# Optimization experiments

Hardware: AMD Instinct MI355X
Metric: run time of the kernel (lower is better)

Reference implementation:

```python
import jax, jax.numpy as jnp
import numpy as np

H = 16  # num_heads
NEG = -1.0e9


def setup_inputs() -> dict:
    key = jax.random.key(0)
    ks = jax.random.split(key, 12)
    B, Q, D, S = 2, 2048, 1024, 512
    sc = 0.02
    return {
        "main_input": jax.random.normal(ks[0], (B, Q, D), jnp.float32),
        "side_input": jax.random.normal(ks[1], (S, D), jnp.float32),
        "att_mask": jax.random.randint(ks[2], (B, Q, Q + S), 0, 2, jnp.int32),
        "Wq": jax.random.normal(ks[3], (D, D), jnp.float32) * sc,
        "bq": jnp.zeros((D,), jnp.float32),
        "Wk": jax.random.normal(ks[4], (D, D), jnp.float32) * sc,
        "bk": jnp.zeros((D,), jnp.float32),
        "Wv": jax.random.normal(ks[5], (D, D), jnp.float32) * sc,
        "bv": jnp.zeros((D,), jnp.float32),
        "Wo": jax.random.normal(ks[6], (D, D), jnp.float32) * sc,
        "bo": jnp.zeros((D,), jnp.float32),
    }


def _heads(x, W, b):
    # x: [..., D] -> [..., H, d]
    y = x @ W + b
    return y.reshape(y.shape[:-1] + (H, y.shape[-1] // H))


def reference(main_input, side_input, att_mask, Wq, bq, Wk, bk, Wv, bv, Wo, bo):
    B, Q, D = main_input.shape
    S = side_input.shape[0]
    d = D // H
    q = _heads(main_input, Wq, bq)          # [B,Q,H,d]
    k = _heads(main_input, Wk, bk)          # [B,Q,H,d]
    v = _heads(main_input, Wv, bv)          # [B,Q,H,d]
    sk = _heads(side_input, Wk, bk)         # [S,H,d] (shared projections)
    sv = _heads(side_input, Wv, bv)         # [S,H,d]
    scores_main = jnp.einsum('bqhd,bkhd->bhqk', q, k)
    scores_side = jnp.einsum('bqhd,khd->bhqk', q, sk)
    scores = jnp.concatenate([scores_main, scores_side], axis=3)  # [B,H,Q,Q+S]
    scores = scores / jnp.sqrt(jnp.asarray(d, scores.dtype))
    adder = NEG * (1.0 - att_mask.astype(scores.dtype))[:, None, :, :]
    probs = jax.nn.softmax(scores + adder, axis=-1)
    out_main = jnp.einsum('bhqk,bkhd->bqhd', probs[..., :Q], v)
    out_side = jnp.einsum('bhqk,khd->bqhd', probs[..., Q:], sv)
    att = (out_main + out_side).reshape(B, Q, D)
    return att @ Wo + bo
```

## Files before the change

### kernel.cpp

```cpp
#include <hip/hip_runtime.h>
#include <cstdint>

typedef short s16x8 __attribute__((ext_vector_type(8)));
typedef short s16x4 __attribute__((ext_vector_type(4)));
typedef unsigned short u16x4 __attribute__((ext_vector_type(4)));
typedef float f32x4 __attribute__((ext_vector_type(4)));
typedef float f32x16 __attribute__((ext_vector_type(16)));
typedef unsigned int u32x4 __attribute__((ext_vector_type(4)));

#define ND 1024
#define NH 16
#define DH 64
#define NQ 2048
#define NL 2560
#define MMAIN 4096
#define MCAT 4608
#define Q_SCALE 0.18033688011112042f

__device__ __forceinline__ unsigned short f2b(float f) {
  unsigned u = __builtin_bit_cast(unsigned, f);
  u += 0x7FFFu + ((u >> 16) & 1u);
  return (unsigned short)(u >> 16);
}

__device__ __forceinline__ void gload16(const void* g, void* l) {
  __builtin_amdgcn_global_load_lds(
      (const __attribute__((address_space(1))) void*)(unsigned long long)(uintptr_t)g,
      (__attribute__((address_space(3))) void*)(unsigned)(uintptr_t)l,
      16, 0, 0);
}

__device__ __forceinline__ f32x4 mfma16(s16x8 a, s16x8 b, f32x4 c) {
  return __builtin_amdgcn_mfma_f32_16x16x32_bf16(a, b, c, 0, 0, 0);
}
__device__ __forceinline__ f32x16 mfma32(s16x8 a, s16x8 b, f32x16 c) {
  return __builtin_amdgcn_mfma_f32_32x32x16_bf16(a, b, c, 0, 0, 0);
}

__device__ __forceinline__ float exp2r(float x) {
  float r;
  asm("v_exp_f32 %0, %1" : "=v"(r) : "v"(x));
  return r;
}

__device__ __forceinline__ int sext_bit(unsigned w, int c) {
#if __has_builtin(__builtin_amdgcn_sbfe)
  return __builtin_amdgcn_sbfe((int)w, c, 1);
#else
  return -(int)((w >> c) & 1u);
#endif
}

__device__ __forceinline__ unsigned cvt_pk_bf16(float lo, float hi) {
  unsigned d;
  asm("v_cvt_pk_bf16_f32 %0, %1, %2" : "=v"(d) : "v"(lo), "v"(hi));
  return d;
}

__device__ __forceinline__ void plane32_swap(unsigned& a, unsigned& b) {
  asm("v_permlane32_swap_b32 %0, %1" : "+v"(a), "+v"(b));
}

__device__ __forceinline__ f32x16 z16() {
  f32x16 v;
#pragma unroll
  for (int i = 0; i < 16; ++i) v[i] = 0.f;
  return v;
}


__global__ __launch_bounds__(256) void k_prep(const float* __restrict__ mainp,
                                              const float* __restrict__ sidep,
                                              const int* __restrict__ mask,
                                              const float* __restrict__ W0,
                                              const float* __restrict__ W1,
                                              const float* __restrict__ W2,
                                              const float* __restrict__ W3,
                                              short* __restrict__ xcat,
                                              short* __restrict__ Wt,
                                              unsigned* __restrict__ pm) {
  __shared__ float T[64][65];
  const int bid = blockIdx.x;
  const int tid = threadIdx.x;
  if (bid < 4608) {
    size_t i4 = ((size_t)bid * 256 + tid) * 4;
    const float* src =
        (i4 < (size_t)MMAIN * ND) ? (mainp + i4) : (sidep + (i4 - (size_t)MMAIN * ND));
    float4 v = *(const float4*)src;
    s16x4 o;
    o[0] = (short)f2b(v.x); o[1] = (short)f2b(v.y);
    o[2] = (short)f2b(v.z); o[3] = (short)f2b(v.w);
    *(s16x4*)(xcat + i4) = o;
  } else if (bid < 4608 + 1024) {
    const int id = bid - 4608;
    const int z = id >> 8, rem = id & 255;
    const float* W = z == 0 ? W0 : z == 1 ? W1 : z == 2 ? W2 : W3;
    short* out = Wt + (size_t)z * (ND * ND);
    const int r = tid >> 2, c0 = (tid & 3) * 16;
    const int k0 = (rem & 15) * 64, n0 = (rem >> 4) * 64;
#pragma unroll
    for (int i = 0; i < 4; ++i) {
      float4 v = *(const float4*)(W + (size_t)(k0 + r) * ND + n0 + c0 + i * 4);
      T[r][c0 + i * 4 + 0] = v.x; T[r][c0 + i * 4 + 1] = v.y;
      T[r][c0 + i * 4 + 2] = v.z; T[r][c0 + i * 4 + 3] = v.w;
    }
    __syncthreads();
    s16x8 o0, o1;
#pragma unroll
    for (int i = 0; i < 8; ++i) o0[i] = (short)f2b(T[c0 + i][r]);
#pragma unroll
    for (int i = 0; i < 8; ++i) o1[i] = (short)f2b(T[c0 + 8 + i][r]);
    *(s16x8*)(out + (size_t)(n0 + r) * ND + k0 + c0) = o0;
    *(s16x8*)(out + (size_t)(n0 + r) * ND + k0 + c0 + 8) = o1;
  } else {
    const int W = (bid - 5632) * 256 + tid;
    const int4* src = (const int4*)(mask + (size_t)W * 32);
    unsigned bits = 0;
#pragma unroll
    for (int i = 0; i < 8; ++i) {
      int4 v = src[i];
      bits |= (unsigned)(v.x & 1) << (i * 4 + 0);
      bits |= (unsigned)(v.y & 1) << (i * 4 + 1);
      bits |= (unsigned)(v.z & 1) << (i * 4 + 2);
      bits |= (unsigned)(v.w & 1) << (i * 4 + 3);
    }
    pm[W] = bits;
  }
}


__global__ __launch_bounds__(256) void k_gemm_qkv(const short* __restrict__ A,
                                                  const short* __restrict__ Bt,
                                                  const float* __restrict__ bqp,
                                                  const float* __restrict__ bkp,
                                                  const float* __restrict__ bvp,
                                                  short* __restrict__ qb,
                                                  short* __restrict__ kb,
                                                  short* __restrict__ vt) {
  __shared__ __align__(16) short As[128 * 64];
  __shared__ __align__(16) short Bs[128 * 64];
  const int tid = threadIdx.x;
  const int w = tid >> 6, l = tid & 63;
  const int lg = l >> 4, li = l & 15;
  const int wr = w >> 1, wc = w & 1;
  const int fid = blockIdx.x + 24 * blockIdx.y;
  const int rid = (fid & 7) * 108 + (fid >> 3);
  const int m0 = (rid / 24) * 128, n0 = (rid % 24) * 128;

  f32x4 acc[4][4];
#pragma unroll
  for (int i = 0; i < 4; ++i)
#pragma unroll
    for (int j = 0; j < 4; ++j) acc[i][j] = (f32x4){0.f, 0.f, 0.f, 0.f};

  const int cb = (l & 7) ^ (l >> 3);
  const int rsub = l >> 3;

  for (int kt = 0; kt < 16; ++kt) {
    __syncthreads();
#pragma unroll
    for (int i = 0; i < 4; ++i) {
      int c = w * 4 + i;
      int rr = c * 8 + rsub;
      gload16(A + (size_t)(m0 + rr) * ND + kt * 64 + cb * 8, As + c * 512);
      gload16(Bt + (size_t)(n0 + rr) * ND + kt * 64 + cb * 8, Bs + c * 512);
    }
    __syncthreads();
#pragma unroll
    for (int kk = 0; kk < 2; ++kk) {
      const int blk = (((kk * 4) + lg) ^ (l & 7)) * 8;
      s16x8 af[4], bf[4];
#pragma unroll
      for (int mf = 0; mf < 4; ++mf)
        af[mf] = *(const s16x8*)(As + (wr * 64 + mf * 16 + li) * 64 + blk);
#pragma unroll
      for (int nf = 0; nf < 4; ++nf)
        bf[nf] = *(const s16x8*)(Bs + (wc * 64 + nf * 16 + li) * 64 + blk);
#pragma unroll
      for (int mf = 0; mf < 4; ++mf)
#pragma unroll
        for (int nf = 0; nf < 4; ++nf)
          acc[mf][nf] = mfma16(af[mf], bf[nf], acc[mf][nf]);
    }
  }

#pragma unroll
  for (int mf = 0; mf < 4; ++mf) {
#pragma unroll
    for (int nf = 0; nf < 4; ++nf) {
      const int n = n0 + wc * 64 + nf * 16 + li;
      const int proj = n >> 10, nn = n & 1023;
      const int h = nn >> 6, dd = nn & 63;
      const float bn = (proj == 0 ? bqp : proj == 1 ? bkp : bvp)[nn];
      const int mbase = m0 + wr * 64 + mf * 16 + lg * 4;
      if (proj == 0) {
        if (mbase < MMAIN) {
#pragma unroll
          for (int r = 0; r < 4; ++r) {
            int m = mbase + r;
            int b = m >> 11, q = m & 2047;
            qb[((size_t)(b * NH + h) * NQ + q) * DH + dd] =
                (short)f2b((acc[mf][nf][r] + bn) * Q_SCALE);
          }
        }
      } else if (proj == 1) {
#pragma unroll
        for (int r = 0; r < 4; ++r) {
          int m = mbase + r;
          short v = (short)f2b(acc[mf][nf][r] + bn);
          if (m < MMAIN) {
            int b = m >> 11, p = m & 2047;
            kb[((size_t)(b * NH + h) * NL + p) * DH + dd] = v;
          } else {
            int p = NQ + (m - MMAIN);
            kb[((size_t)h * NL + p) * DH + dd] = v;
            kb[((size_t)(NH + h) * NL + p) * DH + dd] = v;
          }
        }
      } else {
        u16x4 vv;
#pragma unroll
        for (int r = 0; r < 4; ++r) vv[r] = f2b(acc[mf][nf][r] + bn);
        if (mbase < MMAIN) {
          int b = mbase >> 11, p = mbase & 2047;
          *(u16x4*)(vt + ((size_t)(b * NH + h) * DH + dd) * NL + p) = vv;
        } else {
          int p = NQ + (mbase - MMAIN);
          *(u16x4*)(vt + ((size_t)h * DH + dd) * NL + p) = vv;
          *(u16x4*)(vt + ((size_t)(NH + h) * DH + dd) * NL + p) = vv;
        }
      }
    }
  }
}


__global__ __launch_bounds__(256) void k_gemm_out(const short* __restrict__ A,
                                                  const short* __restrict__ Bt,
                                                  const float* __restrict__ bias,
                                                  float* __restrict__ outp) {
  __shared__ __align__(16) short As[128 * 64];
  __shared__ __align__(16) short Bs[64 * 64];
  const int tid = threadIdx.x;
  const int w = tid >> 6, l = tid & 63;
  const int lg = l >> 4, li = l & 15;
  const int wr = w >> 1, wc = w & 1;
  const int fid = blockIdx.x + 16 * blockIdx.y;
  const int rid = (fid & 7) * 64 + (fid >> 3);
  const int m0 = (rid >> 4) * 128, n0 = (rid & 15) * 64;

  f32x4 acc[4][2];
#pragma unroll
  for (int i = 0; i < 4; ++i)
#pragma unroll
    for (int j = 0; j < 2; ++j) acc[i][j] = (f32x4){0.f, 0.f, 0.f, 0.f};

  const int cb = (l & 7) ^ (l >> 3);
  const int rsub = l >> 3;

  for (int kt = 0; kt < 16; ++kt) {
    __syncthreads();
#pragma unroll
    for (int i = 0; i < 4; ++i) {
      int c = w * 4 + i;
      int rr = c * 8 + rsub;
      gload16(A + (size_t)(m0 + rr) * ND + kt * 64 + cb * 8, As + c * 512);
    }
#pragma unroll
    for (int i = 0; i < 2; ++i) {
      int c = w * 2 + i;
      int rr = c * 8 + rsub;
      gload16(Bt + (size_t)(n0 + rr) * ND + kt * 64 + cb * 8, Bs + c * 512);
    }
    __syncthreads();
#pragma unroll
    for (int kk = 0; kk < 2; ++kk) {
      const int blk = (((kk * 4) + lg) ^ (l & 7)) * 8;
      s16x8 af[4], bf[2];
#pragma unroll
      for (int mf = 0; mf < 4; ++mf)
        af[mf] = *(const s16x8*)(As + (wr * 64 + mf * 16 + li) * 64 + blk);
#pragma unroll
      for (int nf = 0; nf < 2; ++nf)
        bf[nf] = *(const s16x8*)(Bs + (wc * 32 + nf * 16 + li) * 64 + blk);
#pragma unroll
      for (int mf = 0; mf < 4; ++mf)
#pragma unroll
        for (int nf = 0; nf < 2; ++nf)
          acc[mf][nf] = mfma16(af[mf], bf[nf], acc[mf][nf]);
    }
  }

#pragma unroll
  for (int mf = 0; mf < 4; ++mf) {
#pragma unroll
    for (int nf = 0; nf < 2; ++nf) {
      const int n = n0 + wc * 32 + nf * 16 + li;
      const float bn = bias[n];
      const int mbase = m0 + wr * 64 + mf * 16 + lg * 4;
#pragma unroll
      for (int r = 0; r < 4; ++r)
        outp[(size_t)(mbase + r) * ND + n] = acc[mf][nf][r] + bn;
    }
  }
}


#define PROC_TILE(STV, WSV, PB0, PB1)                                        \
  do {                                                                       \
    unsigned pk_[8];                                                         \
    _Pragma("unroll") for (int r_ = 0; r_ < 16; ++r_) {                      \
      const int c_ = (r_ & 3) + 8 * (r_ >> 2);                               \
      float p_ = exp2r(STV[r_]);                                             \
      p_ = __builtin_bit_cast(float, __builtin_bit_cast(unsigned, p_) &      \
                                         (unsigned)sext_bit(WSV, c_));       \
      lr += p_;                                                              \
      STV[r_] = p_;                                                          \
    }                                                                        \
    _Pragma("unroll") for (int m_ = 0; m_ < 8; ++m_)                         \
        pk_[m_] = cvt_pk_bf16(STV[2 * m_], STV[2 * m_ + 1]);                 \
    plane32_swap(pk_[0], pk_[2]);                                            \
    plane32_swap(pk_[1], pk_[3]);                                            \
    plane32_swap(pk_[4], pk_[6]);                                            \
    plane32_swap(pk_[5], pk_[7]);                                            \
    {                                                                        \
      u32x4 t_ = {pk_[0], pk_[1], pk_[2], pk_[3]};                           \
      PB0 = __builtin_bit_cast(s16x8, t_);                                   \
    }                                                                        \
    {                                                                        \
      u32x4 t_ = {pk_[4], pk_[5], pk_[6], pk_[7]};                           \
      PB1 = __builtin_bit_cast(s16x8, t_);                                   \
    }                                                                        \
  } while (0)

#define ATTN_TILE(CUR, T, DONEXT)                                            \
  do {                                                                       \
    unsigned mw_ = pmrow[(T)];                                               \
    if (DONEXT) {                                                            \
      gload16(kg + (size_t)((T) + 1) * 2048, kl + ((CUR) ^ 1) * 4096);       \
      gload16(vg + ((T) + 1) * 32, vl + ((CUR) ^ 1) * 4096);                 \
    }                                                                        \
    f32x16 st_;                                                              \
    __builtin_amdgcn_s_setprio(1);                                           \
    st_ = mfma32(*(const s16x8*)(ldsg + (CUR) * 4096 + koff[0]), qa[0], ZACC); \
    st_ = mfma32(*(const s16x8*)(ldsg + (CUR) * 4096 + koff[1]), qa[1], st_);  \
    st_ = mfma32(*(const s16x8*)(ldsg + (CUR) * 4096 + koff[2]), qa[2], st_);  \
    st_ = mfma32(*(const s16x8*)(ldsg + (CUR) * 4096 + koff[3]), qa[3], st_);  \
    __builtin_amdgcn_s_setprio(0);                                           \
    unsigned ws_ = mw_ >> (hi * 4);                                          \
    s16x8 pb0_, pb1_;                                                        \
    PROC_TILE(st_, ws_, pb0_, pb1_);                                         \
    __builtin_amdgcn_s_setprio(1);                                           \
    {                                                                        \
      s16x8 v0_ = *(const s16x8*)(ldsg + 8192 + (CUR) * 4096 + voff[0]);     \
      s16x8 v1_ =                                                            \
          *(const s16x8*)(ldsg + 8192 + (CUR) * 4096 + voff[0] + 2048);      \
      ot0 = mfma32(v0_, pb0_, ot0);                                          \
      ot1 = mfma32(v1_, pb0_, ot1);                                          \
    }                                                                        \
    {                                                                        \
      s16x8 v0_ = *(const s16x8*)(ldsg + 8192 + (CUR) * 4096 + voff[1]);     \
      s16x8 v1_ =                                                            \
          *(const s16x8*)(ldsg + 8192 + (CUR) * 4096 + voff[1] + 2048);      \
      ot0 = mfma32(v0_, pb1_, ot0);                                          \
      ot1 = mfma32(v1_, pb1_, ot1);                                          \
    }                                                                        \
    __builtin_amdgcn_s_setprio(0);                                           \
    __syncthreads();                                                         \
  } while (0)

__global__ __launch_bounds__(512, 2) void k_attn2(const short* __restrict__ qbuf,
                                                  const short* __restrict__ kbuf,
                                                  const short* __restrict__ vtbuf,
                                                  const unsigned* __restrict__ pmask,
                                                  short* __restrict__ attbuf) {
  __shared__ __align__(16) short lds[16384];
  char* ldsb = (char*)lds;

  const int tid = threadIdx.x;
  const int w = tid >> 6, l = tid & 63;
  const int wg = w & 3, g = w >> 2;
  const int li = l & 31, hi = l >> 5;
  const int bh = blockIdx.x;
  const int b = bh >> 4, h = bh & 15;
  const int qr0 = blockIdx.y * 128 + wg * 32;
  const size_t bhs = (size_t)bh;
  char* ldsg = ldsb + g * 16384;

  s16x8 qa[4];
  {
    const short* qp = qbuf + (bhs * NQ + qr0 + li) * DH + hi * 8;
#pragma unroll
    for (int ks = 0; ks < 4; ++ks) qa[ks] = *(const s16x8*)(qp + ks * 16);
  }

  int koff[4];
#pragma unroll
  for (int ks = 0; ks < 4; ++ks)
    koff[ks] = li * 128 + ((((ks << 1) | hi) ^ (li & 7)) << 4);

  int voff[2];
#pragma unroll
  for (int ks2 = 0; ks2 < 2; ++ks2)
    voff[ks2] = li * 64 + ((((ks2 << 1) | hi) ^ ((li >> 1) & 3)) << 4);

  const short* kg = kbuf + (bhs * NL + g * 1280 + wg * 8 + (l >> 3)) * DH +
                    (((l & 7) ^ (l >> 3)) << 3);
  const short* vg = vtbuf + (bhs * DH + wg * 16 + (l >> 2)) * NL + g * 1280 +
                    (((l & 3) ^ ((l >> 3) & 3)) << 3);
  char* kl = ldsg + wg * 1024;
  char* vl = ldsg + 8192 + wg * 1024;

  const unsigned* pmrow = pmask + ((size_t)b * NQ + qr0 + li) * 80 + g * 40;

  const f32x16 ZACC = z16();
  f32x16 ot0 = z16(), ot1 = z16();
  float lr = 0.f;

  gload16(kg, kl);
  gload16(vg, vl);
  __syncthreads();

  for (int tt = 0; tt < 20; ++tt) {
    const int t0 = 2 * tt;
    ATTN_TILE(0, t0, 1);
    ATTN_TILE(1, t0 + 1, (t0 + 2 < 40));
  }

  lr += __shfl_xor(lr, 32);

  float* comb = (float*)ldsb;
  const int half = wg >> 1;
  const int slot = ((wg & 1) * 64 + l) * 33;
  float lsum = lr;
#pragma unroll
  for (int ph = 0; ph < 2; ++ph) {
    __syncthreads();
    if (g == 1 && half == ph) {
#pragma unroll
      for (int i = 0; i < 16; ++i) comb[slot + i] = ot0[i];
#pragma unroll
      for (int i = 0; i < 16; ++i) comb[slot + 16 + i] = ot1[i];
      comb[slot + 32] = lr;
    }
    __syncthreads();
    if (g == 0 && half == ph) {
#pragma unroll
      for (int i = 0; i < 16; ++i) ot0[i] += comb[slot + i];
#pragma unroll
      for (int i = 0; i < 16; ++i) ot1[i] += comb[slot + 16 + i];
      lsum += comb[slot + 32];
    }
  }
  if (g == 0) {
    const float inv = 1.0f / lsum;
    short* orow = attbuf + ((size_t)b * NQ + qr0 + li) * ND + h * 64;
#pragma unroll
    for (int gg = 0; gg < 4; ++gg) {
      u16x4 v0, v1;
#pragma unroll
      for (int r = 0; r < 4; ++r) {
        v0[r] = f2b(ot0[gg * 4 + r] * inv);
        v1[r] = f2b(ot1[gg * 4 + r] * inv);
      }
      *(u16x4*)(orow + gg * 8 + hi * 4) = v0;
      *(u16x4*)(orow + 32 + gg * 8 + hi * 4) = v1;
    }
  }
}


extern "C" void kernel_launch(void* const* d_in, const int* in_sizes, int n_in,
                              void* d_out, int out_size, void* d_ws, size_t ws_size,
                              hipStream_t stream) {
  const float* mainp = (const float*)d_in[0];
  const float* sidep = (const float*)d_in[1];
  const int* mask = (const int*)d_in[2];
  const float* Wq = (const float*)d_in[3];
  const float* bq = (const float*)d_in[4];
  const float* Wk = (const float*)d_in[5];
  const float* bk = (const float*)d_in[6];
  const float* Wv = (const float*)d_in[7];
  const float* bv = (const float*)d_in[8];
  const float* Wo = (const float*)d_in[9];
  const float* bo = (const float*)d_in[10];

  char* ws = (char*)d_ws;
  short* xcat   = (short*)(ws + 0);
  short* Wt     = (short*)(ws + 9437184);
  short* qbuf   = (short*)(ws + 17825792);
  short* kbuf   = (short*)(ws + 26214400);
  short* vtbuf  = (short*)(ws + 36700160);
  short* attbuf = (short*)(ws + 47185920);
  unsigned* pmask = (unsigned*)(ws + 55574528);

  k_prep<<<6912, 256, 0, stream>>>(mainp, sidep, mask, Wq, Wk, Wv, Wo,
                                   xcat, Wt, pmask);

  k_gemm_qkv<<<dim3(24, 36), 256, 0, stream>>>(xcat, Wt, bq, bk, bv, qbuf, kbuf, vtbuf);

  k_attn2<<<dim3(32, 16), 512, 0, stream>>>(qbuf, kbuf, vtbuf, pmask, attbuf);

  k_gemm_out<<<dim3(16, 32), 256, 0, stream>>>(attbuf, Wt + 3145728, bo, (float*)d_out);
}
```

Measured before the change: 148.7 us.

## Split attention KV range across grid z and fuse partial combine into output GEMM

New measurement: 185.4 us. +24.7%, slower.

```diff
diff --git a/kernel.cpp b/kernel.cpp
--- a/kernel.cpp
+++ b/kernel.cpp
@@ -23,6 +23,10 @@
   return (unsigned short)(u >> 16);
 }
 
+__device__ __forceinline__ float b2f(short s) {
+  return __builtin_bit_cast(float, (unsigned)((unsigned short)s) << 16);
+}
+
 __device__ __forceinline__ void gload16(const void* g, void* l) {
   __builtin_amdgcn_global_load_lds(
       (const __attribute__((address_space(1))) void*)(unsigned long long)(uintptr_t)g,
@@ -40,6 +44,11 @@
 __device__ __forceinline__ float exp2r(float x) {
   float r;
   asm("v_exp_f32 %0, %1" : "=v"(r) : "v"(x));
+  return r;
+}
+__device__ __forceinline__ float rcpr(float x) {
+  float r;
+  asm("v_rcp_f32 %0, %1" : "=v"(r) : "v"(x));
   return r;
 }
 
@@ -235,7 +244,9 @@
 }
 
 
-__global__ __launch_bounds__(256) void k_gemm_out(const short* __restrict__ A,
+__global__ __launch_bounds__(256) void k_gemm_out(const short* __restrict__ opA,
+                                                  const short* __restrict__ opB,
+                                                  const float* __restrict__ lbuf,
                                                   const short* __restrict__ Bt,
                                                   const float* __restrict__ bias,
                                                   float* __restrict__ outp) {
@@ -261,16 +272,32 @@
   for (int kt = 0; kt < 16; ++kt) {
     __syncthreads();
 #pragma unroll
-    for (int i = 0; i < 4; ++i) {
-      int c = w * 4 + i;
-      int rr = c * 8 + rsub;
-      gload16(A + (size_t)(m0 + rr) * ND + kt * 64 + cb * 8, As + c * 512);
-    }
-#pragma unroll
     for (int i = 0; i < 2; ++i) {
       int c = w * 2 + i;
       int rr = c * 8 + rsub;
       gload16(Bt + (size_t)(n0 + rr) * ND + kt * 64 + cb * 8, Bs + c * 512);
+    }
+#pragma unroll
+    for (int i = 0; i < 4; ++i) {
+      int c = w * 4 + i;
+      int rr = c * 8 + rsub;
+      int m = m0 + rr;
+      int b = m >> 11, q = m & 2047;
+      size_t prow = ((size_t)(b * NH + kt)) * NQ + q;
+      float lA = lbuf[prow], lB = lbuf[65536 + prow];
+      float rs = rcpr(lA + lB);
+      float wA = lA * rs, wB = lB * rs;
+      s16x8 a8 = *(const s16x8*)(opA + prow * 64 + cb * 8);
+      s16x8 b8 = *(const s16x8*)(opB + prow * 64 + cb * 8);
+      unsigned pk[4];
+#pragma unroll
+      for (int j = 0; j < 4; ++j) {
+        float f0 = b2f(a8[2 * j]) * wA + b2f(b8[2 * j]) * wB;
+        float f1 = b2f(a8[2 * j + 1]) * wA + b2f(b8[2 * j + 1]) * wB;
+        pk[j] = cvt_pk_bf16(f0, f1);
+      }
+      u32x4 pv = {pk[0], pk[1], pk[2], pk[3]};
+      *(u32x4*)(As + c * 512 + l * 8) = pv;
     }
     __syncthreads();
 #pragma unroll
@@ -373,7 +400,9 @@
                                                   const short* __restrict__ kbuf,
                                                   const short* __restrict__ vtbuf,
                                                   const unsigned* __restrict__ pmask,
-                                                  short* __restrict__ attbuf) {
+                                                  short* __restrict__ opA,
+                                                  short* __restrict__ opB,
+                                                  float* __restrict__ lbuf) {
   __shared__ __align__(16) short lds[16384];
   char* ldsb = (char*)lds;
 
@@ -382,9 +411,11 @@
   const int wg = w & 3, g = w >> 2;
   const int li = l & 31, hi = l >> 5;
   const int bh = blockIdx.x;
-  const int b = bh >> 4, h = bh & 15;
+  const int b = bh >> 4;
+  const int h2 = blockIdx.z;
   const int qr0 = blockIdx.y * 128 + wg * 32;
   const size_t bhs = (size_t)bh;
+  const int kvbase = h2 * 1280 + g * 640;
   char* ldsg = ldsb + g * 16384;
 
   s16x8 qa[4];
@@ -404,14 +435,15 @@
   for (int ks2 = 0; ks2 < 2; ++ks2)
     voff[ks2] = li * 64 + ((((ks2 << 1) | hi) ^ ((li >> 1) & 3)) << 4);
 
-  const short* kg = kbuf + (bhs * NL + g * 1280 + wg * 8 + (l >> 3)) * DH +
+  const short* kg = kbuf + (bhs * NL + kvbase + wg * 8 + (l >> 3)) * DH +
                     (((l & 7) ^ (l >> 3)) << 3);
-  const short* vg = vtbuf + (bhs * DH + wg * 16 + (l >> 2)) * NL + g * 1280 +
+  const short* vg = vtbuf + (bhs * DH + wg * 16 + (l >> 2)) * NL + kvbase +
                     (((l & 3) ^ ((l >> 3) & 3)) << 3);
   char* kl = ldsg + wg * 1024;
   char* vl = ldsg + 8192 + wg * 1024;
 
-  const unsigned* pmrow = pmask + ((size_t)b * NQ + qr0 + li) * 80 + g * 40;
+  const unsigned* pmrow =
+      pmask + ((size_t)b * NQ + qr0 + li) * 80 + h2 * 40 + g * 20;
 
   const f32x16 ZACC = z16();
   f32x16 ot0 = z16(), ot1 = z16();
@@ -421,10 +453,10 @@
   gload16(vg, vl);
   __syncthreads();
 
-  for (int tt = 0; tt < 20; ++tt) {
+  for (int tt = 0; tt < 10; ++tt) {
     const int t0 = 2 * tt;
     ATTN_TILE(0, t0, 1);
-    ATTN_TILE(1, t0 + 1, (t0 + 2 < 40));
+    ATTN_TILE(1, t0 + 1, (t0 + 2 < 20));
   }
 
   lr += __shfl_xor(lr, 32);
@@ -454,7 +486,7 @@
   }
   if (g == 0) {
     const float inv = 1.0f / lsum;
-    short* orow = attbuf + ((size_t)b * NQ + qr0 + li) * ND + h * 64;
+    short* orow = (h2 ? opB : opA) + ((size_t)bh * NQ + qr0 + li) * 64;
 #pragma unroll
     for (int gg = 0; gg < 4; ++gg) {
       u16x4 v0, v1;
@@ -466,6 +498,7 @@
       *(u16x4*)(orow + gg * 8 + hi * 4) = v0;
       *(u16x4*)(orow + 32 + gg * 8 + hi * 4) = v1;
     }
+    if (hi == 0) lbuf[(size_t)h2 * 65536 + bhs * NQ + qr0 + li] = lsum;
   }
 }
 
@@ -491,15 +524,19 @@
   short* qbuf   = (short*)(ws + 17825792);
   short* kbuf   = (short*)(ws + 26214400);
   short* vtbuf  = (short*)(ws + 36700160);
-  short* attbuf = (short*)(ws + 47185920);
+  short* opB    = (short*)(ws + 47185920);
   unsigned* pmask = (unsigned*)(ws + 55574528);
+  short* opA    = (short*)(ws + 0);
+  float* lbuf   = (float*)(ws + 8388608);
 
   k_prep<<<6912, 256, 0, stream>>>(mainp, sidep, mask, Wq, Wk, Wv, Wo,
                                    xcat, Wt, pmask);
 
   k_gemm_qkv<<<dim3(24, 36), 256, 0, stream>>>(xcat, Wt, bq, bk, bv, qbuf, kbuf, vtbuf);
 
-  k_attn2<<<dim3(32, 16), 512, 0, stream>>>(qbuf, kbuf, vtbuf, pmask, attbuf);
-
-  k_gemm_out<<<dim3(16, 32), 256, 0, stream>>>(attbuf, Wt + 3145728, bo, (float*)d_out);
-}
+  k_attn2<<<dim3(32, 16, 2), 512, 0, stream>>>(qbuf, kbuf, vtbuf, pmask,
+                                               opA, opB, lbuf);
+
+  k_gemm_out<<<dim3(16, 32), 256, 0, stream>>>(opA, opB, lbuf,
+                                               Wt + 3145728, bo, (float*)d_out);
+}
```
